# Optimization experiments

Measured on AMD Instinct MI355X. Metric: run time of the kernel, lower is better.

Reference implementation:

```python
import jax, jax.numpy as jnp
import numpy as np

B = 256        # batch size
D = 256        # feature dim
N = 100000     # memory bank size (num pseudo classes)
TEMP = 0.07    # SCT_Memory temperature


def setup_inputs() -> dict:
    key = jax.random.key(0)
    k1, k2, k3 = jax.random.split(key, 3)
    inputs = jax.random.normal(k1, (B, D), dtype=jnp.float32)
    # ReID features are L2-normalized before hitting the memory
    inputs = inputs / jnp.linalg.norm(inputs, axis=1, keepdims=True)
    indexes = jax.random.randint(k2, (B,), 0, N, dtype=jnp.int32)
    features = jax.random.normal(k3, (N, D), dtype=jnp.float32)
    features = features / jnp.linalg.norm(features, axis=1, keepdims=True)
    return {"inputs": inputs, "indexes": indexes, "features": features,
            "momentum": 0.2}


def reference(inputs, indexes, features, momentum):
    # ExemplarMemory.forward: outputs = inputs.mm(features.t())
    # SCT_Memory then scales by 1/temp to form cluster_score.
    out = jnp.matmul(inputs, features.T)  # [B, N]
    return out / TEMP
```

## Files before the change

kernel.cpp:

```cpp
#include <hip/hip_runtime.h>
#include <hip/hip_bf16.h>


typedef __attribute__((ext_vector_type(8))) __bf16 bf16x8;
typedef __attribute__((ext_vector_type(4))) float  floatx4;
typedef __attribute__((ext_vector_type(4))) unsigned int uint4v;

#define NB 100000
#define KD 256
#define BN 64
#define NTILES 1563
#define GRID 512
#define LDS_STRIDE 136

union FragCast { uint4v u; bf16x8 f; };

__device__ __forceinline__ unsigned pk(float a, float b) {
  __hip_bfloat162 h = __float22bfloat162_rn(float2{a, b});
  union { __hip_bfloat162 h2; unsigned u; } c; c.h2 = h; return c.u;
}

__device__ __forceinline__ void barrier_lgkm() {
  asm volatile("s_waitcnt lgkmcnt(0)" ::: "memory");
  __builtin_amdgcn_s_barrier();
  asm volatile("" ::: "memory");
}

__global__ __launch_bounds__(1024, 4)
void sct_gemm(const float* __restrict__ inputs,
              const float* __restrict__ features,
              float* __restrict__ out) {
  __shared__ unsigned lds[BN * LDS_STRIDE];

  const int tid  = threadIdx.x;
  const int ws   = tid >> 6;
  const int lane = tid & 63;
  const int quad = lane >> 4;
  const int l16  = lane & 15;
  const int q4   = quad * 4;

  const int b = blockIdx.x;
  const int ntiles = (NTILES - b + GRID - 1) / GRID;

  const int srow0 = tid >> 5,     sck0 = tid & 31;
  const int srow1 = 32 + srow0,   sck1 = sck0;

  float4 pf0a, pf0b, pf1a, pf1b;
  {
    const int n0 = b * BN;
    pf0a = pf0b = pf1a = pf1b = make_float4(0.f, 0.f, 0.f, 0.f);
    if (n0 + srow0 < NB) {
      const float4* p = (const float4*)(features + (size_t)(n0 + srow0) * KD + sck0 * 8);
      pf0a = p[0]; pf0b = p[1];
    }
    if (n0 + srow1 < NB) {
      const float4* p = (const float4*)(features + (size_t)(n0 + srow1) * KD + sck1 * 8);
      pf1a = p[0]; pf1b = p[1];
    }
  }

  const float scale = 1.0f / 0.07f;
  bf16x8 afrag[8];
  {
    const float* arow = inputs + (ws * 16 + l16) * KD + quad * 8;
    #pragma unroll
    for (int t = 0; t < 8; ++t) {
      const float4* p = (const float4*)(arow + t * 32);
      const float4 a0 = p[0], a1 = p[1];
      FragCast fc;
      fc.u.x = pk(a0.x * scale, a0.y * scale);
      fc.u.y = pk(a0.z * scale, a0.w * scale);
      fc.u.z = pk(a1.x * scale, a1.y * scale);
      fc.u.w = pk(a1.z * scale, a1.w * scale);
      afrag[t] = fc.f;
    }
  }

  float* const orow = out + (size_t)(ws * 16 + l16) * NB;

  for (int it = 0; it < ntiles; ++it) {
    const int n0 = (b + it * GRID) * BN;

    barrier_lgkm();

    {
      uint4v w;
      w.x = pk(pf0a.x, pf0a.y); w.y = pk(pf0a.z, pf0a.w);
      w.z = pk(pf0b.x, pf0b.y); w.w = pk(pf0b.z, pf0b.w);
      *(uint4v*)&lds[srow0 * LDS_STRIDE + sck0 * 4] = w;
      w.x = pk(pf1a.x, pf1a.y); w.y = pk(pf1a.z, pf1a.w);
      w.z = pk(pf1b.x, pf1b.y); w.w = pk(pf1b.z, pf1b.w);
      *(uint4v*)&lds[srow1 * LDS_STRIDE + sck1 * 4] = w;
    }

    barrier_lgkm();

    if (it + 1 < ntiles) {
      const int nn0 = (b + (it + 1) * GRID) * BN;
      pf0a = pf0b = pf1a = pf1b = make_float4(0.f, 0.f, 0.f, 0.f);
      if (nn0 + srow0 < NB) {
        const float4* p = (const float4*)(features + (size_t)(nn0 + srow0) * KD + sck0 * 8);
        pf0a = p[0]; pf0b = p[1];
      }
      if (nn0 + srow1 < NB) {
        const float4* p = (const float4*)(features + (size_t)(nn0 + srow1) * KD + sck1 * 8);
        pf1a = p[0]; pf1b = p[1];
      }
    }

    floatx4 acc[4];
    #pragma unroll
    for (int nt = 0; nt < 4; ++nt) acc[nt] = floatx4{0.f, 0.f, 0.f, 0.f};

    #pragma unroll
    for (int t = 0; t < 8; ++t) {
      #pragma unroll
      for (int nt = 0; nt < 4; ++nt) {
        FragCast fc;
        fc.u = *(const uint4v*)&lds[(nt * 16 + l16) * LDS_STRIDE + t * 16 + q4];
        acc[nt] = __builtin_amdgcn_mfma_f32_16x16x32_bf16(fc.f, afrag[t], acc[nt], 0, 0, 0);
      }
    }

    #pragma unroll
    for (int nt = 0; nt < 4; ++nt) {
      const int n = n0 + nt * 16 + q4;
      if (n < NB)
        __builtin_nontemporal_store(acc[nt], (floatx4*)(orow + n));
    }
  }
}

extern "C" void kernel_launch(void* const* d_in, const int* in_sizes, int n_in,
                              void* d_out, int out_size, void* d_ws, size_t ws_size,
                              hipStream_t stream) {
  const float* inputs   = (const float*)d_in[0];
  const float* features = (const float*)d_in[2];
  float* out = (float*)d_out;

  sct_gemm<<<GRID, 1024, 0, stream>>>(inputs, features, out);
}
```

Baseline: 210.1 us.

## Double-buffer LDS with XOR swizzle, two-deep prefetch, halve grid

Replaces the padded single LDS tile with a double-buffered, XOR-swizzled layout. This removes one barrier per iteration and lets the next tile's LDS write overlap the current MFMA work, with global loads now prefetched two tiles ahead. The grid is halved to 256 blocks so each block handles more tiles, and output stores switch from nontemporal to ordinary stores. In exchange it uses twice the LDS, keeps live registers longer, and the smaller grid may underfill the GPU.

```diff
diff --git a/kernel.cpp b/kernel.cpp
--- a/kernel.cpp
+++ b/kernel.cpp
@@ -10,8 +10,8 @@
 #define KD 256
 #define BN 64
 #define NTILES 1563
-#define GRID 512
-#define LDS_STRIDE 136
+#define GRID 256
+#define NCHUNK 32
 
 union FragCast { uint4v u; bf16x8 f; };
 
@@ -30,7 +30,7 @@
 void sct_gemm(const float* __restrict__ inputs,
               const float* __restrict__ features,
               float* __restrict__ out) {
-  __shared__ unsigned lds[BN * LDS_STRIDE];
+  __shared__ uint4v lds[2][BN][NCHUNK];
 
   const int tid  = threadIdx.x;
   const int ws   = tid >> 6;
@@ -38,23 +38,26 @@
   const int quad = lane >> 4;
   const int l16  = lane & 15;
   const int q4   = quad * 4;
+  const int e3   = l16 & 7;
 
   const int b = blockIdx.x;
   const int ntiles = (NTILES - b + GRID - 1) / GRID;
 
-  const int srow0 = tid >> 5,     sck0 = tid & 31;
-  const int srow1 = 32 + srow0,   sck1 = sck0;
+  const int srow0 = tid >> 5, sck = tid & 31;
+  const int srow1 = 32 + srow0;
+  const int wch0 = sck ^ (srow0 & 7);
+  const int wch1 = sck ^ (srow1 & 7);
 
   float4 pf0a, pf0b, pf1a, pf1b;
   {
     const int n0 = b * BN;
     pf0a = pf0b = pf1a = pf1b = make_float4(0.f, 0.f, 0.f, 0.f);
     if (n0 + srow0 < NB) {
-      const float4* p = (const float4*)(features + (size_t)(n0 + srow0) * KD + sck0 * 8);
+      const float4* p = (const float4*)(features + (size_t)(n0 + srow0) * KD + sck * 8);
       pf0a = p[0]; pf0b = p[1];
     }
     if (n0 + srow1 < NB) {
-      const float4* p = (const float4*)(features + (size_t)(n0 + srow1) * KD + sck1 * 8);
+      const float4* p = (const float4*)(features + (size_t)(n0 + srow1) * KD + sck * 8);
       pf1a = p[0]; pf1b = p[1];
     }
   }
@@ -76,34 +79,55 @@
     }
   }
 
+  {
+    uint4v w;
+    w.x = pk(pf0a.x, pf0a.y); w.y = pk(pf0a.z, pf0a.w);
+    w.z = pk(pf0b.x, pf0b.y); w.w = pk(pf0b.z, pf0b.w);
+    lds[0][srow0][wch0] = w;
+    w.x = pk(pf1a.x, pf1a.y); w.y = pk(pf1a.z, pf1a.w);
+    w.z = pk(pf1b.x, pf1b.y); w.w = pk(pf1b.z, pf1b.w);
+    lds[0][srow1][wch1] = w;
+  }
+  if (1 < ntiles) {
+    const int nn0 = (b + GRID) * BN;
+    pf0a = pf0b = pf1a = pf1b = make_float4(0.f, 0.f, 0.f, 0.f);
+    if (nn0 + srow0 < NB) {
+      const float4* p = (const float4*)(features + (size_t)(nn0 + srow0) * KD + sck * 8);
+      pf0a = p[0]; pf0b = p[1];
+    }
+    if (nn0 + srow1 < NB) {
+      const float4* p = (const float4*)(features + (size_t)(nn0 + srow1) * KD + sck * 8);
+      pf1a = p[0]; pf1b = p[1];
+    }
+  }
+
   float* const orow = out + (size_t)(ws * 16 + l16) * NB;
 
   for (int it = 0; it < ntiles; ++it) {
     const int n0 = (b + it * GRID) * BN;
-
-    barrier_lgkm();
-
-    {
-      uint4v w;
-      w.x = pk(pf0a.x, pf0a.y); w.y = pk(pf0a.z, pf0a.w);
-      w.z = pk(pf0b.x, pf0b.y); w.w = pk(pf0b.z, pf0b.w);
-      *(uint4v*)&lds[srow0 * LDS_STRIDE + sck0 * 4] = w;
-      w.x = pk(pf1a.x, pf1a.y); w.y = pk(pf1a.z, pf1a.w);
-      w.z = pk(pf1b.x, pf1b.y); w.w = pk(pf1b.z, pf1b.w);
-      *(uint4v*)&lds[srow1 * LDS_STRIDE + sck1 * 4] = w;
-    }
+    const int cb = it & 1, nb = cb ^ 1;
 
     barrier_lgkm();
 
     if (it + 1 < ntiles) {
-      const int nn0 = (b + (it + 1) * GRID) * BN;
+      uint4v w;
+      w.x = pk(pf0a.x, pf0a.y); w.y = pk(pf0a.z, pf0a.w);
+      w.z = pk(pf0b.x, pf0b.y); w.w = pk(pf0b.z, pf0b.w);
+      lds[nb][srow0][wch0] = w;
+      w.x = pk(pf1a.x, pf1a.y); w.y = pk(pf1a.z, pf1a.w);
+      w.z = pk(pf1b.x, pf1b.y); w.w = pk(pf1b.z, pf1b.w);
+      lds[nb][srow1][wch1] = w;
+    }
+
+    if (it + 2 < ntiles) {
+      const int nn0 = (b + (it + 2) * GRID) * BN;
       pf0a = pf0b = pf1a = pf1b = make_float4(0.f, 0.f, 0.f, 0.f);
       if (nn0 + srow0 < NB) {
-        const float4* p = (const float4*)(features + (size_t)(nn0 + srow0) * KD + sck0 * 8);
+        const float4* p = (const float4*)(features + (size_t)(nn0 + srow0) * KD + sck * 8);
         pf0a = p[0]; pf0b = p[1];
       }
       if (nn0 + srow1 < NB) {
-        const float4* p = (const float4*)(features + (size_t)(nn0 + srow1) * KD + sck1 * 8);
+        const float4* p = (const float4*)(features + (size_t)(nn0 + srow1) * KD + sck * 8);
         pf1a = p[0]; pf1b = p[1];
       }
     }
@@ -117,7 +141,7 @@
       #pragma unroll
       for (int nt = 0; nt < 4; ++nt) {
         FragCast fc;
-        fc.u = *(const uint4v*)&lds[(nt * 16 + l16) * LDS_STRIDE + t * 16 + q4];
+        fc.u = lds[cb][nt * 16 + l16][(t * 4 + quad) ^ e3];
         acc[nt] = __builtin_amdgcn_mfma_f32_16x16x32_bf16(fc.f, afrag[t], acc[nt], 0, 0, 0);
       }
     }
@@ -126,7 +150,7 @@
     for (int nt = 0; nt < 4; ++nt) {
       const int n = n0 + nt * 16 + q4;
       if (n < NB)
-        __builtin_nontemporal_store(acc[nt], (floatx4*)(orow + n));
+        *(floatx4*)(orow + n) = acc[nt];
     }
   }
 }
```

After: 199.1 us. 5.3% less time.

## Double N tile to 128, XOR-swizzle LDS, and use plain output stores

Applied to the files above, without the earlier changes.

Raises the per-block tile from 64 to 128 feature rows and halves the grid to 256 blocks. Each thread now loads a contiguous 128-byte row segment, and the padded LDS layout is replaced by an XOR-swizzled layout to avoid bank conflicts. Output stores switch from nontemporal to ordinary stores. The larger tile amortizes barriers and prefetch over more MFMA work, but it raises register pressure (eight float4 prefetch registers and eight accumulators) and leaves fewer blocks to hide latency.

```diff
diff --git a/kernel.cpp b/kernel.cpp
--- a/kernel.cpp
+++ b/kernel.cpp
@@ -8,10 +8,10 @@
 
 #define NB 100000
 #define KD 256
-#define BN 64
-#define NTILES 1563
-#define GRID 512
-#define LDS_STRIDE 136
+#define BN 128
+#define NTILES 782
+#define GRID 256
+#define NCHUNK 32
 
 union FragCast { uint4v u; bf16x8 f; };
 
@@ -30,7 +30,7 @@
 void sct_gemm(const float* __restrict__ inputs,
               const float* __restrict__ features,
               float* __restrict__ out) {
-  __shared__ unsigned lds[BN * LDS_STRIDE];
+  __shared__ uint4v lds[BN][NCHUNK];
 
   const int tid  = threadIdx.x;
   const int ws   = tid >> 6;
@@ -38,24 +38,23 @@
   const int quad = lane >> 4;
   const int l16  = lane & 15;
   const int q4   = quad * 4;
+  const int e3   = l16 & 7;
 
   const int b = blockIdx.x;
   const int ntiles = (NTILES - b + GRID - 1) / GRID;
 
-  const int srow0 = tid >> 5,     sck0 = tid & 31;
-  const int srow1 = 32 + srow0,   sck1 = sck0;
+  const int srow = tid >> 3, sk = tid & 7;
+  const int rswz = srow & 7;
 
-  float4 pf0a, pf0b, pf1a, pf1b;
+  float4 pf[8];
   {
     const int n0 = b * BN;
-    pf0a = pf0b = pf1a = pf1b = make_float4(0.f, 0.f, 0.f, 0.f);
-    if (n0 + srow0 < NB) {
-      const float4* p = (const float4*)(features + (size_t)(n0 + srow0) * KD + sck0 * 8);
-      pf0a = p[0]; pf0b = p[1];
-    }
-    if (n0 + srow1 < NB) {
-      const float4* p = (const float4*)(features + (size_t)(n0 + srow1) * KD + sck1 * 8);
-      pf1a = p[0]; pf1b = p[1];
+    #pragma unroll
+    for (int j = 0; j < 8; ++j) pf[j] = make_float4(0.f, 0.f, 0.f, 0.f);
+    if (n0 + srow < NB) {
+      const float4* p = (const float4*)(features + (size_t)(n0 + srow) * KD + sk * 32);
+      #pragma unroll
+      for (int j = 0; j < 8; ++j) pf[j] = p[j];
     }
   }
 
@@ -84,49 +83,49 @@
     barrier_lgkm();
 
     {
-      uint4v w;
-      w.x = pk(pf0a.x, pf0a.y); w.y = pk(pf0a.z, pf0a.w);
-      w.z = pk(pf0b.x, pf0b.y); w.w = pk(pf0b.z, pf0b.w);
-      *(uint4v*)&lds[srow0 * LDS_STRIDE + sck0 * 4] = w;
-      w.x = pk(pf1a.x, pf1a.y); w.y = pk(pf1a.z, pf1a.w);
-      w.z = pk(pf1b.x, pf1b.y); w.w = pk(pf1b.z, pf1b.w);
-      *(uint4v*)&lds[srow1 * LDS_STRIDE + sck1 * 4] = w;
+      #pragma unroll
+      for (int j = 0; j < 4; ++j) {
+        uint4v w;
+        w.x = pk(pf[2 * j].x, pf[2 * j].y);
+        w.y = pk(pf[2 * j].z, pf[2 * j].w);
+        w.z = pk(pf[2 * j + 1].x, pf[2 * j + 1].y);
+        w.w = pk(pf[2 * j + 1].z, pf[2 * j + 1].w);
+        lds[srow][(sk * 4 + j) ^ rswz] = w;
+      }
     }
 
     barrier_lgkm();
 
     if (it + 1 < ntiles) {
       const int nn0 = (b + (it + 1) * GRID) * BN;
-      pf0a = pf0b = pf1a = pf1b = make_float4(0.f, 0.f, 0.f, 0.f);
-      if (nn0 + srow0 < NB) {
-        const float4* p = (const float4*)(features + (size_t)(nn0 + srow0) * KD + sck0 * 8);
-        pf0a = p[0]; pf0b = p[1];
-      }
-      if (nn0 + srow1 < NB) {
-        const float4* p = (const float4*)(features + (size_t)(nn0 + srow1) * KD + sck1 * 8);
-        pf1a = p[0]; pf1b = p[1];
+      #pragma unroll
+      for (int j = 0; j < 8; ++j) pf[j] = make_float4(0.f, 0.f, 0.f, 0.f);
+      if (nn0 + srow < NB) {
+        const float4* p = (const float4*)(features + (size_t)(nn0 + srow) * KD + sk * 32);
+        #pragma unroll
+        for (int j = 0; j < 8; ++j) pf[j] = p[j];
       }
     }
 
-    floatx4 acc[4];
+    floatx4 acc[8];
     #pragma unroll
-    for (int nt = 0; nt < 4; ++nt) acc[nt] = floatx4{0.f, 0.f, 0.f, 0.f};
+    for (int nt = 0; nt < 8; ++nt) acc[nt] = floatx4{0.f, 0.f, 0.f, 0.f};
 
     #pragma unroll
     for (int t = 0; t < 8; ++t) {
       #pragma unroll
-      for (int nt = 0; nt < 4; ++nt) {
+      for (int nt = 0; nt < 8; ++nt) {
         FragCast fc;
-        fc.u = *(const uint4v*)&lds[(nt * 16 + l16) * LDS_STRIDE + t * 16 + q4];
+        fc.u = lds[nt * 16 + l16][(t * 4 + quad) ^ e3];
         acc[nt] = __builtin_amdgcn_mfma_f32_16x16x32_bf16(fc.f, afrag[t], acc[nt], 0, 0, 0);
       }
     }
 
     #pragma unroll
-    for (int nt = 0; nt < 4; ++nt) {
+    for (int nt = 0; nt < 8; ++nt) {
       const int n = n0 + nt * 16 + q4;
       if (n < NB)
-        __builtin_nontemporal_store(acc[nt], (floatx4*)(orow + n));
+        *(floatx4*)(orow + n) = acc[nt];
     }
   }
 }
```

Result: no change. 214.2 us (+2.0%).

## Split batch rows across two block halves with 512-thread blocks

Applied to the files above, without the earlier changes.

Blocks shrink from 1024 to 512 threads, and the grid is split so each half of the blocks computes 128 of the 256 batch rows over 256 column groups. Each feature tile is therefore loaded and converted twice, once per M-half, but each thread prefetches four rows and the blocks are smaller, which may improve scheduling and occupancy. The change also raises wave priority around the MFMA loop and replaces nontemporal output stores with ordinary stores. The cost is doubled feature reads and bf16 conversion work.

```diff
diff --git a/kernel.cpp b/kernel.cpp
--- a/kernel.cpp
+++ b/kernel.cpp
@@ -11,6 +11,7 @@
 #define BN 64
 #define NTILES 1563
 #define GRID 512
+#define BLK 512
 #define LDS_STRIDE 136
 
 union FragCast { uint4v u; bf16x8 f; };
@@ -26,7 +27,7 @@
   asm volatile("" ::: "memory");
 }
 
-__global__ __launch_bounds__(1024, 4)
+__global__ __launch_bounds__(BLK, 4)
 void sct_gemm(const float* __restrict__ inputs,
               const float* __restrict__ features,
               float* __restrict__ out) {
@@ -39,30 +40,30 @@
   const int l16  = lane & 15;
   const int q4   = quad * 4;
 
-  const int b = blockIdx.x;
-  const int ntiles = (NTILES - b + GRID - 1) / GRID;
+  const int g  = blockIdx.x & 255;
+  const int mh = blockIdx.x >> 8;
+  const int ntiles = (NTILES - g + 255) / 256;
 
-  const int srow0 = tid >> 5,     sck0 = tid & 31;
-  const int srow1 = 32 + srow0,   sck1 = sck0;
+  const int srow = tid >> 5, sck = tid & 31;
 
-  float4 pf0a, pf0b, pf1a, pf1b;
+  float4 pfa[4], pfb[4];
   {
-    const int n0 = b * BN;
-    pf0a = pf0b = pf1a = pf1b = make_float4(0.f, 0.f, 0.f, 0.f);
-    if (n0 + srow0 < NB) {
-      const float4* p = (const float4*)(features + (size_t)(n0 + srow0) * KD + sck0 * 8);
-      pf0a = p[0]; pf0b = p[1];
-    }
-    if (n0 + srow1 < NB) {
-      const float4* p = (const float4*)(features + (size_t)(n0 + srow1) * KD + sck1 * 8);
-      pf1a = p[0]; pf1b = p[1];
+    const int n0 = g * BN;
+    #pragma unroll
+    for (int j = 0; j < 4; ++j) {
+      pfa[j] = pfb[j] = make_float4(0.f, 0.f, 0.f, 0.f);
+      const int r = srow + j * 16;
+      if (n0 + r < NB) {
+        const float4* p = (const float4*)(features + (size_t)(n0 + r) * KD + sck * 8);
+        pfa[j] = p[0]; pfb[j] = p[1];
+      }
     }
   }
 
   const float scale = 1.0f / 0.07f;
   bf16x8 afrag[8];
   {
-    const float* arow = inputs + (ws * 16 + l16) * KD + quad * 8;
+    const float* arow = inputs + (mh * 128 + ws * 16 + l16) * KD + quad * 8;
     #pragma unroll
     for (int t = 0; t < 8; ++t) {
       const float4* p = (const float4*)(arow + t * 32);
@@ -76,35 +77,35 @@
     }
   }
 
-  float* const orow = out + (size_t)(ws * 16 + l16) * NB;
+  float* const orow = out + (size_t)(mh * 128 + ws * 16 + l16) * NB;
 
   for (int it = 0; it < ntiles; ++it) {
-    const int n0 = (b + it * GRID) * BN;
+    const int n0 = (g + it * 256) * BN;
 
     barrier_lgkm();
 
     {
-      uint4v w;
-      w.x = pk(pf0a.x, pf0a.y); w.y = pk(pf0a.z, pf0a.w);
-      w.z = pk(pf0b.x, pf0b.y); w.w = pk(pf0b.z, pf0b.w);
-      *(uint4v*)&lds[srow0 * LDS_STRIDE + sck0 * 4] = w;
-      w.x = pk(pf1a.x, pf1a.y); w.y = pk(pf1a.z, pf1a.w);
-      w.z = pk(pf1b.x, pf1b.y); w.w = pk(pf1b.z, pf1b.w);
-      *(uint4v*)&lds[srow1 * LDS_STRIDE + sck1 * 4] = w;
+      #pragma unroll
+      for (int j = 0; j < 4; ++j) {
+        uint4v w;
+        w.x = pk(pfa[j].x, pfa[j].y); w.y = pk(pfa[j].z, pfa[j].w);
+        w.z = pk(pfb[j].x, pfb[j].y); w.w = pk(pfb[j].z, pfb[j].w);
+        *(uint4v*)&lds[(srow + j * 16) * LDS_STRIDE + sck * 4] = w;
+      }
     }
 
     barrier_lgkm();
 
     if (it + 1 < ntiles) {
-      const int nn0 = (b + (it + 1) * GRID) * BN;
-      pf0a = pf0b = pf1a = pf1b = make_float4(0.f, 0.f, 0.f, 0.f);
-      if (nn0 + srow0 < NB) {
-        const float4* p = (const float4*)(features + (size_t)(nn0 + srow0) * KD + sck0 * 8);
-        pf0a = p[0]; pf0b = p[1];
-      }
-      if (nn0 + srow1 < NB) {
-        const float4* p = (const float4*)(features + (size_t)(nn0 + srow1) * KD + sck1 * 8);
-        pf1a = p[0]; pf1b = p[1];
+      const int nn0 = (g + (it + 1) * 256) * BN;
+      #pragma unroll
+      for (int j = 0; j < 4; ++j) {
+        pfa[j] = pfb[j] = make_float4(0.f, 0.f, 0.f, 0.f);
+        const int r = srow + j * 16;
+        if (nn0 + r < NB) {
+          const float4* p = (const float4*)(features + (size_t)(nn0 + r) * KD + sck * 8);
+          pfa[j] = p[0]; pfb[j] = p[1];
+        }
       }
     }
 
@@ -112,6 +113,7 @@
     #pragma unroll
     for (int nt = 0; nt < 4; ++nt) acc[nt] = floatx4{0.f, 0.f, 0.f, 0.f};
 
+    __builtin_amdgcn_s_setprio(1);
     #pragma unroll
     for (int t = 0; t < 8; ++t) {
       #pragma unroll
@@ -121,12 +123,13 @@
         acc[nt] = __builtin_amdgcn_mfma_f32_16x16x32_bf16(fc.f, afrag[t], acc[nt], 0, 0, 0);
       }
     }
+    __builtin_amdgcn_s_setprio(0);
 
     #pragma unroll
     for (int nt = 0; nt < 4; ++nt) {
       const int n = n0 + nt * 16 + q4;
       if (n < NB)
-        __builtin_nontemporal_store(acc[nt], (floatx4*)(orow + n));
+        *(floatx4*)(orow + n) = acc[nt];
     }
   }
 }
@@ -138,5 +141,5 @@
   const float* features = (const float*)d_in[2];
   float* out = (float*)d_out;
 
-  sct_gemm<<<GRID, 1024, 0, stream>>>(inputs, features, out);
+  sct_gemm<<<GRID, BLK, 0, stream>>>(inputs, features, out);
 }
```

Measured after the change: 207.0 us. About the same (-1.5%).
